# Kernel tuning notes

Measured on AMD Instinct MI355X. Metric: run time of the kernel, lower is better.

## Reference

```python
import jax, jax.numpy as jnp
import numpy as np

IN_F = 4096
OUT_F = 4096
BLOCK = 16      # weight values decoded per latent code
D_LAT = 16      # latent dim per code
HID = 64        # decoder hidden width
K = 65536       # codebook size
NB = IN_F * OUT_F // BLOCK  # 1,048,576 blocks


def setup_inputs() -> dict:
    key = jax.random.key(0)
    ks = jax.random.split(key, 10)
    return {
        "x": jax.random.normal(ks[0], (4, 2048, IN_F), jnp.float32),
        "y_in_idx": jax.random.randint(ks[1], (NB,), 0, K),
        "codebook": jax.random.normal(ks[2], (K, D_LAT), jnp.float32) * 0.1,
        "W1": jax.random.normal(ks[3], (D_LAT, HID), jnp.float32) * 0.1,
        "b1": jnp.zeros((HID,), jnp.float32),
        "W2": jax.random.normal(ks[4], (HID, BLOCK), jnp.float32) * 0.1,
        "b2": jnp.zeros((BLOCK,), jnp.float32),
        "scale": jax.random.uniform(ks[5], (OUT_F,), jnp.float32, 0.5, 1.5),
        "shift": jax.random.normal(ks[6], (OUT_F,), jnp.float32) * 0.01,
        "bias": jax.random.normal(ks[7], (OUT_F,), jnp.float32) * 0.02,
    }


def reference(x, y_in_idx, codebook, W1, b1, W2, b2, scale, shift, bias):
    # 1) gather latent codes for every weight block: [NB, D_LAT]
    codes = codebook[y_in_idx]
    # 2) decode latents -> weight blocks via small MLP (comp_W_from_y analogue)
    h = jax.nn.relu(codes @ W1 + b1)          # [NB, HID]
    blocks = h @ W2 + b2                      # [NB, BLOCK]
    # 3) assemble reconstructed (standardized) weight hatWr: [OUT_F, IN_F]
    Wr = blocks.reshape(OUT_F, IN_F)
    # 4) de-standardize with per-output-row metadata (de_standardize_Wr)
    W_hat = Wr * scale[:, None] + shift[:, None]
    # 5) F.linear(input, W_hat, bias): [B, S, OUT_F]
    return jnp.einsum('bsi,oi->bso', x, W_hat) + bias
```

## Files before the change

kernel.cpp:

```cpp
#include <hip/hip_runtime.h>
#include <hip/hip_bf16.h>

#define IN_F   4096
#define OUT_F  4096
#define HID    64
#define D_LAT  16
#define BLK    16
#define NB     (IN_F * OUT_F / BLK)
#define M_TOT  8192
#define K_TOT  IN_F
#define N_TOT  OUT_F

typedef __bf16 bf16x8 __attribute__((ext_vector_type(8)));
typedef float  f32x4  __attribute__((ext_vector_type(4)));

__global__ __launch_bounds__(256) void convert_x_kernel(
    const float* __restrict__ x, __hip_bfloat16* __restrict__ xb) {
  size_t i = ((size_t)blockIdx.x * 256 + threadIdx.x) * 8;
  const float4* p = (const float4*)(x + i);
  float4 a = p[0], b = p[1];
  union { __hip_bfloat16 h[8]; uint4 q; } u;
  u.h[0] = __float2bfloat16(a.x); u.h[1] = __float2bfloat16(a.y);
  u.h[2] = __float2bfloat16(a.z); u.h[3] = __float2bfloat16(a.w);
  u.h[4] = __float2bfloat16(b.x); u.h[5] = __float2bfloat16(b.y);
  u.h[6] = __float2bfloat16(b.z); u.h[7] = __float2bfloat16(b.w);
  *(uint4*)(xb + i) = u.q;
}

__global__ __launch_bounds__(256) void decode_mfma_kernel(
    const int* __restrict__ yidx, const float* __restrict__ codebook,
    const float* __restrict__ W1, const float* __restrict__ b1,
    const float* __restrict__ W2, const float* __restrict__ b2,
    const float* __restrict__ scale, const float* __restrict__ shift,
    __hip_bfloat16* __restrict__ What) {
  __shared__ __align__(16) __hip_bfloat16 sH[4][16 * 72];
  const int lane = threadIdx.x & 63;
  const int wave = threadIdx.x >> 6;
  const int n = lane & 15;
  const int q = lane >> 4;
  const bool act = q < 2;

  union { __hip_bfloat16 h[8]; bf16x8 v; } uz;
#pragma unroll
  for (int j = 0; j < 8; j++) uz.h[j] = __float2bfloat16(0.f);
  const bf16x8 zf = uz.v;
  const f32x4 z4 = (f32x4){0.f, 0.f, 0.f, 0.f};

  bf16x8 frag1[4];
#pragma unroll
  for (int g = 0; g < 4; g++) {
    union { __hip_bfloat16 h[8]; bf16x8 v; } u;
#pragma unroll
    for (int j = 0; j < 8; j++) {
      int k = (q * 8 + j) & 15;
      float w = act ? W1[k * HID + g * 16 + n] : 0.f;
      u.h[j] = __float2bfloat16(w);
    }
    frag1[g] = u.v;
  }
  bf16x8 frag2[2];
#pragma unroll
  for (int kk = 0; kk < 2; kk++) {
    union { __hip_bfloat16 h[8]; bf16x8 v; } u;
#pragma unroll
    for (int j = 0; j < 8; j++)
      u.h[j] = __float2bfloat16(W2[(kk * 32 + q * 8 + j) * BLK + n]);
    frag2[kk] = u.v;
  }
  float b1v[4];
#pragma unroll
  for (int g = 0; g < 4; g++) b1v[g] = b1[g * 16 + n];
  const float b2v = b2[n];

  const int c0w = blockIdx.x * 256 + wave * 64;
#pragma unroll 1
  for (int i = 0; i < 4; i++) {
    const int cbase = c0w + i * 16;
    const int id = yidx[cbase + n];
    const float4* cp = (const float4*)(codebook + (size_t)id * D_LAT + (q & 1) * 8);
    float4 ca = cp[0], cb = cp[1];
    union { __hip_bfloat16 h[8]; bf16x8 v; } ua;
    ua.h[0] = __float2bfloat16(ca.x); ua.h[1] = __float2bfloat16(ca.y);
    ua.h[2] = __float2bfloat16(ca.z); ua.h[3] = __float2bfloat16(ca.w);
    ua.h[4] = __float2bfloat16(cb.x); ua.h[5] = __float2bfloat16(cb.y);
    ua.h[6] = __float2bfloat16(cb.z); ua.h[7] = __float2bfloat16(cb.w);
    bf16x8 afrag = act ? ua.v : zf;

    f32x4 hC[4];
#pragma unroll
    for (int g = 0; g < 4; g++)
      hC[g] = __builtin_amdgcn_mfma_f32_16x16x32_bf16(afrag, frag1[g], z4, 0, 0, 0);

    __syncthreads();
#pragma unroll
    for (int g = 0; g < 4; g++)
#pragma unroll
      for (int r = 0; r < 4; r++) {
        float hv = fmaxf(hC[g][r] + b1v[g], 0.f);
        sH[wave][(q * 4 + r) * 72 + g * 16 + n] = __float2bfloat16(hv);
      }
    __syncthreads();

    bf16x8 a2_0 = *(const bf16x8*)&sH[wave][n * 72 + q * 8];
    bf16x8 a2_1 = *(const bf16x8*)&sH[wave][n * 72 + 32 + q * 8];
    f32x4 o4 = __builtin_amdgcn_mfma_f32_16x16x32_bf16(a2_0, frag2[0], z4, 0, 0, 0);
    o4 = __builtin_amdgcn_mfma_f32_16x16x32_bf16(a2_1, frag2[1], o4, 0, 0, 0);

    const int o = cbase >> 8;
    const float sc = scale[o], sh = shift[o];
#pragma unroll
    for (int r = 0; r < 4; r++) {
      int code = cbase + q * 4 + r;
      What[(size_t)code * BLK + n] = __float2bfloat16((o4[r] + b2v) * sc + sh);
    }
  }
}

__device__ inline void gload_lds16(const void* g, void* l) {
  __builtin_amdgcn_global_load_lds(
      (const __attribute__((address_space(1))) void*)g,
      (__attribute__((address_space(3))) void*)l, 16, 0, 0);
}

__global__ __launch_bounds__(256, 2) void gemm_bt_kernel(
    const __hip_bfloat16* __restrict__ A, const __hip_bfloat16* __restrict__ B,
    const float* __restrict__ bias, float* __restrict__ C) {
  __shared__ __align__(16) __hip_bfloat16 sA[256 * 32];
  __shared__ __align__(16) __hip_bfloat16 sB[128 * 32];
  const int lane = threadIdx.x & 63;
  const int wave = threadIdx.x >> 6;
  const int m0 = blockIdx.y * 256;
  const int n0 = blockIdx.x * 128;
  const int wr = wave >> 1;
  const int wc = wave & 1;

  const int srow = lane >> 2;
  const int schk = (lane & 3) ^ ((lane >> 3) & 3);
  const __hip_bfloat16* aSrc =
      A + (size_t)(m0 + wave * 64 + srow) * K_TOT + schk * 8;
  const __hip_bfloat16* bSrc =
      B + (size_t)(n0 + wave * 32 + srow) * K_TOT + schk * 8;

  const int fl = lane & 15;
  const int pos = (lane >> 4) ^ ((fl >> 1) & 3);
  const __hip_bfloat16* aRd = &sA[(wr * 128 + fl) * 32 + pos * 8];
  const __hip_bfloat16* bRd = &sB[(wc * 64 + fl) * 32 + pos * 8];

  f32x4 acc[8][4];
#pragma unroll
  for (int i = 0; i < 8; i++)
#pragma unroll
    for (int j = 0; j < 4; j++) acc[i][j] = (f32x4){0.f, 0.f, 0.f, 0.f};

  for (int k0 = 0; k0 < K_TOT; k0 += 32) {
#pragma unroll
    for (int i = 0; i < 4; i++)
      gload_lds16(aSrc + (size_t)i * 16 * K_TOT + k0,
                  (char*)sA + (wave * 4 + i) * 1024);
#pragma unroll
    for (int i = 0; i < 2; i++)
      gload_lds16(bSrc + (size_t)i * 16 * K_TOT + k0,
                  (char*)sB + (wave * 2 + i) * 1024);
    __syncthreads();

    bf16x8 bf[4];
#pragma unroll
    for (int nt = 0; nt < 4; nt++) bf[nt] = *(const bf16x8*)(bRd + nt * 16 * 32);
#pragma unroll
    for (int mt = 0; mt < 8; mt++) {
      bf16x8 af = *(const bf16x8*)(aRd + mt * 16 * 32);
#pragma unroll
      for (int nt = 0; nt < 4; nt++)
        acc[mt][nt] = __builtin_amdgcn_mfma_f32_16x16x32_bf16(
            af, bf[nt], acc[mt][nt], 0, 0, 0);
    }
    __syncthreads();
  }

  float bs[4];
#pragma unroll
  for (int nt = 0; nt < 4; nt++) bs[nt] = bias[n0 + wc * 64 + nt * 16 + fl];
#pragma unroll
  for (int mt = 0; mt < 8; mt++) {
    int r0 = m0 + wr * 128 + mt * 16 + (lane >> 4) * 4;
#pragma unroll
    for (int nt = 0; nt < 4; nt++) {
      int cn = n0 + wc * 64 + nt * 16 + fl;
#pragma unroll
      for (int r = 0; r < 4; r++)
        C[(size_t)(r0 + r) * N_TOT + cn] = acc[mt][nt][r] + bs[nt];
    }
  }
}

extern "C" void kernel_launch(void* const* d_in, const int* in_sizes, int n_in,
                              void* d_out, int out_size, void* d_ws, size_t ws_size,
                              hipStream_t stream) {
  const float* x        = (const float*)d_in[0];
  const int*   yidx     = (const int*)d_in[1];
  const float* codebook = (const float*)d_in[2];
  const float* W1       = (const float*)d_in[3];
  const float* b1       = (const float*)d_in[4];
  const float* W2       = (const float*)d_in[5];
  const float* b2       = (const float*)d_in[6];
  const float* scale    = (const float*)d_in[7];
  const float* shift    = (const float*)d_in[8];
  const float* bias     = (const float*)d_in[9];
  float* out = (float*)d_out;

  __hip_bfloat16* What = (__hip_bfloat16*)d_ws;
  __hip_bfloat16* xb   = (__hip_bfloat16*)((char*)d_ws + (size_t)32 * 1024 * 1024);

  convert_x_kernel<<<(M_TOT * (size_t)K_TOT) / (256 * 8), 256, 0, stream>>>(x, xb);
  decode_mfma_kernel<<<NB / 256, 256, 0, stream>>>(yidx, codebook, W1, b1, W2, b2,
                                                   scale, shift, What);
  gemm_bt_kernel<<<dim3(N_TOT / 128, M_TOT / 256), 256, 0, stream>>>(xb, What, bias, out);
}
```

Measured before the change: 549.1 us.

## Decode codebook once into a lookup table, then gather and de-standardize per block

```diff
diff --git a/kernel.cpp b/kernel.cpp
--- a/kernel.cpp
+++ b/kernel.cpp
@@ -7,6 +7,7 @@
 #define D_LAT  16
 #define BLK    16
 #define NB     (IN_F * OUT_F / BLK)
+#define NCODES 65536
 #define M_TOT  8192
 #define K_TOT  IN_F
 #define N_TOT  OUT_F
@@ -27,12 +28,11 @@
   *(uint4*)(xb + i) = u.q;
 }
 
-__global__ __launch_bounds__(256) void decode_mfma_kernel(
-    const int* __restrict__ yidx, const float* __restrict__ codebook,
+__global__ __launch_bounds__(256) void decode_table_kernel(
+    const float* __restrict__ codebook,
     const float* __restrict__ W1, const float* __restrict__ b1,
     const float* __restrict__ W2, const float* __restrict__ b2,
-    const float* __restrict__ scale, const float* __restrict__ shift,
-    __hip_bfloat16* __restrict__ What) {
+    float* __restrict__ table) {
   __shared__ __align__(16) __hip_bfloat16 sH[4][16 * 72];
   const int lane = threadIdx.x & 63;
   const int wave = threadIdx.x >> 6;
@@ -76,7 +76,7 @@
 #pragma unroll 1
   for (int i = 0; i < 4; i++) {
     const int cbase = c0w + i * 16;
-    const int id = yidx[cbase + n];
+    const int id = cbase + n;
     const float4* cp = (const float4*)(codebook + (size_t)id * D_LAT + (q & 1) * 8);
     float4 ca = cp[0], cb = cp[1];
     union { __hip_bfloat16 h[8]; bf16x8 v; } ua;
@@ -106,14 +106,44 @@
     f32x4 o4 = __builtin_amdgcn_mfma_f32_16x16x32_bf16(a2_0, frag2[0], z4, 0, 0, 0);
     o4 = __builtin_amdgcn_mfma_f32_16x16x32_bf16(a2_1, frag2[1], o4, 0, 0, 0);
 
-    const int o = cbase >> 8;
-    const float sc = scale[o], sh = shift[o];
 #pragma unroll
     for (int r = 0; r < 4; r++) {
       int code = cbase + q * 4 + r;
-      What[(size_t)code * BLK + n] = __float2bfloat16((o4[r] + b2v) * sc + sh);
-    }
-  }
+      table[(size_t)code * BLK + n] = o4[r] + b2v;
+    }
+  }
+}
+
+__global__ __launch_bounds__(256) void gather_scale_kernel(
+    const int* __restrict__ yidx, const float* __restrict__ table,
+    const float* __restrict__ scale, const float* __restrict__ shift,
+    __hip_bfloat16* __restrict__ What) {
+  const int b = blockIdx.x * 256 + threadIdx.x;
+  const int o = blockIdx.x;
+  const float sc = scale[o], sh = shift[o];
+  const int id = yidx[b];
+  const float4* t = (const float4*)(table + (size_t)id * BLK);
+  float4 v0 = t[0], v1 = t[1], v2 = t[2], v3 = t[3];
+  union { __hip_bfloat16 h[16]; uint4 q[2]; } u;
+  u.h[0]  = __float2bfloat16(v0.x * sc + sh);
+  u.h[1]  = __float2bfloat16(v0.y * sc + sh);
+  u.h[2]  = __float2bfloat16(v0.z * sc + sh);
+  u.h[3]  = __float2bfloat16(v0.w * sc + sh);
+  u.h[4]  = __float2bfloat16(v1.x * sc + sh);
+  u.h[5]  = __float2bfloat16(v1.y * sc + sh);
+  u.h[6]  = __float2bfloat16(v1.z * sc + sh);
+  u.h[7]  = __float2bfloat16(v1.w * sc + sh);
+  u.h[8]  = __float2bfloat16(v2.x * sc + sh);
+  u.h[9]  = __float2bfloat16(v2.y * sc + sh);
+  u.h[10] = __float2bfloat16(v2.z * sc + sh);
+  u.h[11] = __float2bfloat16(v2.w * sc + sh);
+  u.h[12] = __float2bfloat16(v3.x * sc + sh);
+  u.h[13] = __float2bfloat16(v3.y * sc + sh);
+  u.h[14] = __float2bfloat16(v3.z * sc + sh);
+  u.h[15] = __float2bfloat16(v3.w * sc + sh);
+  uint4* dst = (uint4*)(What + (size_t)b * BLK);
+  dst[0] = u.q[0];
+  dst[1] = u.q[1];
 }
 
 __device__ inline void gload_lds16(const void* g, void* l) {
@@ -209,10 +239,12 @@
   float* out = (float*)d_out;
 
   __hip_bfloat16* What = (__hip_bfloat16*)d_ws;
+  float* table = (float*)((char*)d_ws + (size_t)32 * 1024 * 1024);
   __hip_bfloat16* xb   = (__hip_bfloat16*)((char*)d_ws + (size_t)32 * 1024 * 1024);
 
+  decode_table_kernel<<<NCODES / 256, 256, 0, stream>>>(codebook, W1, b1, W2, b2,
+                                                        table);
+  gather_scale_kernel<<<NB / 256, 256, 0, stream>>>(yidx, table, scale, shift, What);
   convert_x_kernel<<<(M_TOT * (size_t)K_TOT) / (256 * 8), 256, 0, stream>>>(x, xb);
-  decode_mfma_kernel<<<NB / 256, 256, 0, stream>>>(yidx, codebook, W1, b1, W2, b2,
-                                                   scale, shift, What);
   gemm_bt_kernel<<<dim3(N_TOT / 128, M_TOT / 256), 256, 0, stream>>>(xb, What, bias, out);
 }
```

Result: faster. 530.1 us (-3.5%).
